# Performance work log

Hardware: AMD Instinct MI355X
Metric: run time of the kernel (lower is better)

## Reference

```python
import jax, jax.numpy as jnp
import numpy as np

D_MODEL = 1024
H = 16
D_K = D_MODEL // H  # 64
B, S = 2, 2048


def setup_inputs() -> dict:
    key = jax.random.key(0)
    ks = jax.random.split(key, 8)
    scale = 1.0 / np.sqrt(D_MODEL)
    return {
        "q": jax.random.normal(ks[0], (B, S, D_MODEL), dtype=jnp.float32),
        "k": jax.random.normal(ks[1], (B, S, D_MODEL), dtype=jnp.float32),
        "v": jax.random.normal(ks[2], (B, S, D_MODEL), dtype=jnp.float32),
        "W_q": jax.random.normal(ks[3], (H, D_MODEL, D_K), dtype=jnp.float32) * scale,
        "W_k": jax.random.normal(ks[4], (H, D_MODEL, D_K), dtype=jnp.float32) * scale,
        "W_v": jax.random.normal(ks[5], (H, D_MODEL, D_K), dtype=jnp.float32) * scale,
        "W_o": jax.random.normal(ks[6], (D_MODEL, H * D_K), dtype=jnp.float32) * scale,
        "b_o": jnp.zeros((D_MODEL,), dtype=jnp.float32),
    }


def reference(q, k, v, W_q, W_k, W_v, W_o, b_o):
    b, s, _ = q.shape
    h, _, d_k = W_q.shape
    inv_sqrt_dk = jnp.asarray(1.0 / np.sqrt(d_k), q.dtype)
    # per-head projections: [b, h, s, d_k]
    qh = jnp.einsum("bsd,hdk->bhsk", q, W_q)
    kh = jnp.einsum("bsd,hdk->bhsk", k, W_k)
    vh = jnp.einsum("bsd,hdk->bhsk", v, W_v)
    # scaled dot product attention
    scores = jnp.einsum("bhqk,bhsk->bhqs", qh, kh) * inv_sqrt_dk  # [b,h,S,S]
    attn = jax.nn.softmax(scores, axis=-1)
    ctx = jnp.einsum("bhqs,bhsk->bhqk", attn, vh)  # [b,h,S,d_k]
    # chunk over heads + concat along feature dim -> [b, S, h*d_k], head-major
    ctx = ctx.transpose(0, 2, 1, 3).reshape(b, s, h * d_k)
    # final linear
    return ctx @ W_o.T + b_o
```

## Files before the change

### kernel.cpp

```cpp
#include <hip/hip_runtime.h>
#include <cstdint>
#include <cstddef>


typedef unsigned short bf16_t;
typedef __attribute__((ext_vector_type(8))) short short8;
typedef __attribute__((ext_vector_type(4))) float f32x4;
typedef __attribute__((ext_vector_type(16))) float f32x16;
typedef __attribute__((ext_vector_type(2))) unsigned int uint2v;

__device__ __forceinline__ uint32_t fbits(float f) {
  union { float f; uint32_t u; } v; v.f = f; return v.u;
}
__device__ __forceinline__ bf16_t f2bf(float f) {
  uint32_t u = fbits(f);
  return (bf16_t)((u + 0x7FFFu + ((u >> 16) & 1u)) >> 16);
}
__device__ __forceinline__ uint32_t packbf2(float lo, float hi) {
  uint32_t a = fbits(hi) + 0x8000u;
  uint32_t b = fbits(lo) + 0x8000u;
  return __builtin_amdgcn_perm(a, b, 0x07060302u);
}
__device__ __forceinline__ int4 cvt8(f32x4 lo, f32x4 hi) {
  return make_int4((int)packbf2(lo.x, lo.y), (int)packbf2(lo.z, lo.w),
                   (int)packbf2(hi.x, hi.y), (int)packbf2(hi.z, hi.w));
}

__device__ __forceinline__ void gload16(const bf16_t* g, bf16_t* l) {
  __builtin_amdgcn_global_load_lds(
      (const __attribute__((address_space(1))) void*)g,
      (__attribute__((address_space(3))) void*)l, 16, 0, 0);
}

__global__ void prep_kernel(const float* __restrict__ Wo,
                            const float* __restrict__ Wq, const float* __restrict__ Wk,
                            const float* __restrict__ Wv,
                            const float* __restrict__ q, const float* __restrict__ k,
                            const float* __restrict__ v,
                            bf16_t* __restrict__ Woo,
                            bf16_t* __restrict__ Wtq, bf16_t* __restrict__ Wtk,
                            bf16_t* __restrict__ Wtv,
                            bf16_t* __restrict__ qb, bf16_t* __restrict__ kb,
                            bf16_t* __restrict__ vb) {
  int blk = blockIdx.x;
  int tid = threadIdx.x;
  if (blk < 1024) {
    int i = blk * 256 + tid;
    f32x4 val = ((const f32x4*)Wo)[i];
    ushort4 o;
    o.x = f2bf(val.x); o.y = f2bf(val.y); o.z = f2bf(val.z); o.w = f2bf(val.w);
    ((ushort4*)Woo)[i] = o;
  } else if (blk < 2560) {
    int blk2 = blk - 1024;
    int z = blk2 >> 9, t = blk2 & 511;
    const float* W = z == 0 ? Wq : z == 1 ? Wk : Wv;
    bf16_t* Wt = z == 0 ? Wtq : z == 1 ? Wtk : Wtv;
    int h = t >> 5, d0 = (t & 31) * 32;
    __shared__ float tile[32][65];
    const float* src = W + ((size_t)h << 16) + (size_t)d0 * 64;
    int d = tid >> 3;
#pragma unroll
    for (int j = 0; j < 2; j++) {
      int dk = (tid & 7) * 8 + j * 4;
      *(f32x4*)&tile[d][dk] = *(const f32x4*)(src + d * 64 + dk);
    }
    __syncthreads();
    int dk2 = tid >> 2, c = tid & 3;
    union { ushort s[8]; int4 v; } o;
#pragma unroll
    for (int j = 0; j < 8; j++) o.s[j] = f2bf(tile[c * 8 + j][dk2]);
    *(int4*)(Wt + (size_t)(h * 64 + dk2) * 1024 + d0 + c * 8) = o.v;
  } else {
    int blk3 = blk - 2560;
    int z = blk3 >> 11;
    int t3 = blk3 & 2047;
    const float* src = z == 0 ? q : z == 1 ? k : v;
    bf16_t* dst = z == 0 ? qb : z == 1 ? kb : vb;
    int i = t3 * 256 + tid;
    f32x4 lo = ((const f32x4*)src)[i * 2];
    f32x4 hi = ((const f32x4*)src)[i * 2 + 1];
    ((int4*)dst)[i] = cvt8(lo, hi);
  }
}

__global__ __launch_bounds__(256) void gemm_proj_kernel(
    const bf16_t* __restrict__ A0, const bf16_t* __restrict__ A1, const bf16_t* __restrict__ A2,
    const bf16_t* __restrict__ B0, const bf16_t* __restrict__ B1, const bf16_t* __restrict__ B2,
    bf16_t* __restrict__ O0, bf16_t* __restrict__ O1, bf16_t* __restrict__ O2,
    float s0)
{
  const int bid = blockIdx.x;
  const int nIdx = bid / 96;
  const int g = bid - nIdx * 96;
  const int z = g % 3;
  const int m0 = (g / 3) * 128, n0 = nIdx * 128;

  const bf16_t* A  = z == 0 ? A0 : z == 1 ? A1 : A2;
  const bf16_t* Bt = z == 0 ? B0 : z == 1 ? B1 : B2;
  bf16_t* Cout     = z == 0 ? O0 : z == 1 ? O1 : O2;
  const float scale = z == 0 ? s0 : 1.0f;
  const int K = 1024;

  __shared__ alignas(16) bf16_t smem[18432];

  const int tid = threadIdx.x;
  const int lane = tid & 63, wave = tid >> 6;
  const int wm = wave >> 1, wn = wave & 1;
  const int quad = lane >> 4, l15 = lane & 15;

  f32x4 acc[4][4];
#pragma unroll
  for (int i = 0; i < 4; i++)
#pragma unroll
    for (int j = 0; j < 4; j++) acc[i][j] = (f32x4)0.0f;

  const int srow = tid >> 2, scol = (tid & 3) * 8;
  const bf16_t* pa0 = A  + (size_t)(m0 + srow) * K + scol;
  const bf16_t* pa1 = pa0 + (size_t)64 * K;
  const bf16_t* pb0 = Bt + (size_t)(n0 + srow) * K + scol;
  const bf16_t* pb1 = pb0 + (size_t)64 * K;
  const int lws = wave * 512;

  gload16(pa0, smem + lws);
  gload16(pa1, smem + 2048 + lws);
  gload16(pb0, smem + 4096 + lws);
  gload16(pb1, smem + 6144 + lws);
  __syncthreads();

  for (int it = 0; it < 32; ++it) {
    const int cur = (it & 1) * 8192;
    if (it < 31) {
      const int nxt = ((it + 1) & 1) * 8192;
      const int ko = (it + 1) * 32;
      gload16(pa0 + ko, smem + nxt + lws);
      gload16(pa1 + ko, smem + nxt + 2048 + lws);
      gload16(pb0 + ko, smem + nxt + 4096 + lws);
      gload16(pb1 + ko, smem + nxt + 6144 + lws);
    }

    short8 af[4], bfr[4];
#pragma unroll
    for (int mi = 0; mi < 4; mi++)
      af[mi] = *(const short8*)(smem + cur + (wm * 64 + mi * 16 + l15) * 32 + quad * 8);
#pragma unroll
    for (int ni = 0; ni < 4; ni++)
      bfr[ni] = *(const short8*)(smem + cur + 4096 + (wn * 64 + ni * 16 + l15) * 32 + quad * 8);
#pragma unroll
    for (int mi = 0; mi < 4; mi++)
#pragma unroll
      for (int ni = 0; ni < 4; ni++)
        acc[mi][ni] = __builtin_amdgcn_mfma_f32_16x16x32_bf16(af[mi], bfr[ni], acc[mi][ni], 0, 0, 0);

    __syncthreads();
  }

  const int s0r = m0 & 2047, bb = m0 >> 11, hp = n0 >> 6;
  if (z < 2) {
    bf16_t* slot = smem + wn * 9216;
#pragma unroll
    for (int ni = 0; ni < 4; ni++)
#pragma unroll
      for (int mi = 0; mi < 4; mi++)
#pragma unroll
        for (int r = 0; r < 4; r++)
          slot[(wm * 64 + mi * 16 + quad * 4 + r) * 72 + ni * 16 + l15] =
              f2bf(acc[mi][ni][r] * scale);
    __syncthreads();
#pragma unroll
    for (int rd = 0; rd < 8; ++rd) {
      int idx = rd * 256 + tid;
      int si = idx >> 10, mm = (idx >> 3) & 127, c8 = idx & 7;
      int4 val = *(const int4*)(smem + si * 9216 + mm * 72 + c8 * 8);
      size_t head = (size_t)(bb * 16 + hp + si);
      if (z == 0) {
        *(int4*)(Cout + (head * 2048 + s0r + mm) * 64 + c8 * 8) = val;
      } else {
        int row = s0r + mm;
        int tile = row >> 6, loc = row & 63;
        int f = (loc >> 5) * 4 + (c8 >> 1);
        int j = (c8 & 1) * 32 + (loc & 31);
        *(int4*)(Cout + head * 131072 + (size_t)tile * 4096 + f * 512 + j * 8) = val;
      }
    }
  } else {
    bf16_t* slot = smem + wn * 8704;
#pragma unroll
    for (int ni = 0; ni < 4; ni++)
#pragma unroll
      for (int mi = 0; mi < 4; mi++) {
        uint2 pk = make_uint2(packbf2(acc[mi][ni][0], acc[mi][ni][1]),
                              packbf2(acc[mi][ni][2], acc[mi][ni][3]));
        *(uint2*)(slot + (ni * 16 + l15) * 136 + wm * 64 + mi * 16 + quad * 4) = pk;
      }
    __syncthreads();
#pragma unroll
    for (int rd = 0; rd < 8; ++rd) {
      int idx = rd * 256 + tid;
      int si = idx >> 10, c = (idx >> 4) & 63, ck = idx & 15;
      int4 val = *(const int4*)(smem + si * 8704 + c * 136 + ck * 8);
      int kk = s0r + ck * 8;
      int tile = kk >> 6;
      int f = (c >> 5) * 4 + ((kk >> 4) & 3);
      int j = ((kk >> 3) & 1) * 32 + (c & 31);
      *(int4*)(Cout + (size_t)(bb * 16 + hp + si) * 131072 + (size_t)tile * 4096 + f * 512 + j * 8) = val;
    }
  }
}

__global__ __launch_bounds__(256) void gemm_out_kernel(
    const bf16_t* __restrict__ A, const bf16_t* __restrict__ Bt,
    float* __restrict__ C, const float* __restrict__ bias)
{
  const int K = 1024, N = 1024;
  __shared__ alignas(16) bf16_t smem[12288];
  const int tid = threadIdx.x;
  const int lane = tid & 63, wave = tid >> 6;
  const int quad = lane >> 4, l15 = lane & 15;
  const int m0 = (blockIdx.x & 31) * 128, n0 = (blockIdx.x >> 5) * 64;

  f32x4 acc[2][4];
#pragma unroll
  for (int i = 0; i < 2; i++)
#pragma unroll
    for (int j = 0; j < 4; j++) acc[i][j] = (f32x4)0.0f;

  const int srow = tid >> 2, scol = (tid & 3) * 8;
  const bf16_t* pa0 = A  + (size_t)(m0 + srow) * K + scol;
  const bf16_t* pa1 = pa0 + (size_t)64 * K;
  const bf16_t* pb  = Bt + (size_t)(n0 + srow) * K + scol;
  const int lws = wave * 512;

  gload16(pa0, smem + lws);
  gload16(pa1, smem + 2048 + lws);
  gload16(pb,  smem + 4096 + lws);
  __syncthreads();

  for (int it = 0; it < 32; ++it) {
    const int cur = (it & 1) * 6144;
    if (it < 31) {
      const int nxt = ((it + 1) & 1) * 6144;
      const int ko = (it + 1) * 32;
      gload16(pa0 + ko, smem + nxt + lws);
      gload16(pa1 + ko, smem + nxt + 2048 + lws);
      gload16(pb + ko,  smem + nxt + 4096 + lws);
    }

    short8 af[2], bfr[4];
#pragma unroll
    for (int mi = 0; mi < 2; mi++)
      af[mi] = *(const short8*)(smem + cur + (wave * 32 + mi * 16 + l15) * 32 + quad * 8);
#pragma unroll
    for (int ni = 0; ni < 4; ni++)
      bfr[ni] = *(const short8*)(smem + cur + 4096 + (ni * 16 + l15) * 32 + quad * 8);
#pragma unroll
    for (int mi = 0; mi < 2; mi++)
#pragma unroll
      for (int ni = 0; ni < 4; ni++)
        acc[mi][ni] = __builtin_amdgcn_mfma_f32_16x16x32_bf16(af[mi], bfr[ni], acc[mi][ni], 0, 0, 0);

    __syncthreads();
  }

#pragma unroll
  for (int ni = 0; ni < 4; ni++) {
    int col = n0 + ni * 16 + l15;
    float bv = bias[col];
#pragma unroll
    for (int mi = 0; mi < 2; mi++) {
      int row = m0 + wave * 32 + mi * 16 + quad * 4;
#pragma unroll
      for (int r = 0; r < 4; r++)
        C[(size_t)(row + r) * N + col] = acc[mi][ni][r] + bv;
    }
  }
}

__global__ __launch_bounds__(256) void flash_kernel(
    const bf16_t* __restrict__ qh, const bf16_t* __restrict__ kh,
    const bf16_t* __restrict__ vh, bf16_t* __restrict__ ctx)
{
  __shared__ alignas(16) bf16_t smem[16384];
  const int tid = threadIdx.x, lane = tid & 63, wave = tid >> 6;
  const int hlf = lane >> 5, l31 = lane & 31;
  const int gid = blockIdx.x;
  const int hb = gid & 31;
  const int h = hb & 15, b = hb >> 4;
  const int q0 = (gid >> 5) * 128;
  const size_t headoff = (size_t)hb * 131072;
  const bf16_t* Q  = qh + headoff;
  const bf16_t* Kf = kh + headoff;
  const bf16_t* Vf = vh + headoff;

  short8 qf[4];
#pragma unroll
  for (int dk = 0; dk < 4; dk++)
    qf[dk] = *(const short8*)(Q + (size_t)(q0 + wave * 32 + l31) * 64 + dk * 16 + hlf * 8);

  f32x16 Oa = (f32x16)0.0f, Ob = (f32x16)0.0f;
  float lsum = 0.0f;

  const bf16_t* Kp0 = Kf + tid * 8;
  const bf16_t* Kp1 = Kf + tid * 8 + 2048;
  const bf16_t* Vp0 = Vf + 4096 - 4096 + tid * 8;
  const bf16_t* Vp1 = Vf + tid * 8 + 2048;
  bf16_t* sK = smem + tid * 8;
  bf16_t* sV = smem + 4096 + tid * 8;

  auto body = [&](int buf) {
    const bf16_t* Kb = smem + buf * 8192;
    const bf16_t* Vb = smem + buf * 8192 + 4096;
    f32x16 S0 = (f32x16)0.0f, S1 = (f32x16)0.0f;
#pragma unroll
    for (int dk = 0; dk < 4; dk++) {
      short8 kf0 = *(const short8*)(Kb + dk * 512 + lane * 8);
      short8 kf1 = *(const short8*)(Kb + (4 + dk) * 512 + lane * 8);
      S0 = __builtin_amdgcn_mfma_f32_32x32x16_bf16(kf0, qf[dk], S0, 0, 0, 0);
      S1 = __builtin_amdgcn_mfma_f32_32x32x16_bf16(kf1, qf[dk], S1, 0, 0, 0);
    }
#pragma unroll
    for (int r = 0; r < 16; r++) {
      S0[r] = __builtin_amdgcn_exp2f(S0[r]);
      S1[r] = __builtin_amdgcn_exp2f(S1[r]);
    }
    {
      f32x16 ss = S0 + S1;
      float a0 = (ss[0] + ss[1]) + (ss[2] + ss[3]);
      float a1 = (ss[4] + ss[5]) + (ss[6] + ss[7]);
      float a2 = (ss[8] + ss[9]) + (ss[10] + ss[11]);
      float a3 = (ss[12] + ss[13]) + (ss[14] + ss[15]);
      lsum += (a0 + a1) + (a2 + a3);
    }
#pragma unroll
    for (int mi = 0; mi < 2; mi++) {
      f32x16 P = mi ? S1 : S0;
#pragma unroll
      for (int ksl = 0; ksl < 2; ksl++) {
        const int ks = mi * 2 + ksl, base = ksl * 8;
        uint32_t X = packbf2(P[base + 0], P[base + 1]);
        uint32_t Y = packbf2(P[base + 2], P[base + 3]);
        uint32_t Z = packbf2(P[base + 4], P[base + 5]);
        uint32_t W = packbf2(P[base + 6], P[base + 7]);
        uint2v r1 = __builtin_amdgcn_permlane32_swap(X, Z, false, false);
        uint2v r2 = __builtin_amdgcn_permlane32_swap(Y, W, false, false);
        int4 bi = make_int4((int)r1.x, (int)r2.x, (int)r1.y, (int)r2.y);
        short8 Bf = *(short8*)&bi;
        short8 vf0 = *(const short8*)(Vb + ks * 512 + lane * 8);
        short8 vf1 = *(const short8*)(Vb + (4 + ks) * 512 + lane * 8);
        Oa = __builtin_amdgcn_mfma_f32_32x32x16_bf16(vf0, Bf, Oa, 0, 0, 0);
        Ob = __builtin_amdgcn_mfma_f32_32x32x16_bf16(vf1, Bf, Ob, 0, 0, 0);
      }
    }
  };

  int4 k0a = *(const int4*)Kp0, k0b = *(const int4*)Kp1;
  int4 v0a = *(const int4*)Vp0, v0b = *(const int4*)Vp1;
  *(int4*)sK = k0a; *(int4*)(sK + 2048) = k0b;
  *(int4*)sV = v0a; *(int4*)(sV + 2048) = v0b;
  int4 kAa = *(const int4*)(Kp0 + 4096), kAb = *(const int4*)(Kp1 + 4096);
  int4 vAa = *(const int4*)(Vp0 + 4096), vAb = *(const int4*)(Vp1 + 4096);
  __syncthreads();

  for (int it = 0; it < 32; it += 2) {
    *(int4*)(sK + 8192) = kAa; *(int4*)(sK + 8192 + 2048) = kAb;
    *(int4*)(sV + 8192) = vAa; *(int4*)(sV + 8192 + 2048) = vAb;
    int4 kBa, kBb, vBa, vBb;
    if (it + 2 < 32) {
      kBa = *(const int4*)(Kp0 + (size_t)(it + 2) * 4096);
      kBb = *(const int4*)(Kp1 + (size_t)(it + 2) * 4096);
      vBa = *(const int4*)(Vp0 + (size_t)(it + 2) * 4096);
      vBb = *(const int4*)(Vp1 + (size_t)(it + 2) * 4096);
    }
    body(0);
    __syncthreads();

    if (it + 2 < 32) {
      *(int4*)sK = kBa; *(int4*)(sK + 2048) = kBb;
      *(int4*)sV = vBa; *(int4*)(sV + 2048) = vBb;
    }
    if (it + 3 < 32) {
      kAa = *(const int4*)(Kp0 + (size_t)(it + 3) * 4096);
      kAb = *(const int4*)(Kp1 + (size_t)(it + 3) * 4096);
      vAa = *(const int4*)(Vp0 + (size_t)(it + 3) * 4096);
      vAb = *(const int4*)(Vp1 + (size_t)(it + 3) * 4096);
    }
    body(1);
    __syncthreads();
  }

  lsum += __shfl_xor(lsum, 32, 64);
  float inv = 1.0f / lsum;
  bf16_t* slot = smem + wave * 2048;
  const int swz = l31 & 7;
#pragma unroll
  for (int dmi = 0; dmi < 2; dmi++) {
    f32x16 Ov = dmi ? Ob : Oa;
#pragma unroll
    for (int rq = 0; rq < 4; rq++) {
      uint2 pk = make_uint2(packbf2(Ov[rq * 4 + 0] * inv, Ov[rq * 4 + 1] * inv),
                            packbf2(Ov[rq * 4 + 2] * inv, Ov[rq * 4 + 3] * inv));
      int c = dmi * 4 + rq;
      *(uint2*)(slot + l31 * 64 + ((c ^ swz) * 8 + 4 * hlf)) = pk;
    }
  }
  __syncthreads();
#pragma unroll
  for (int p = 0; p < 4; p++) {
    int s2 = p * 64 + lane;
    int qr = s2 >> 3, cr = s2 & 7;
    int4 val = *(const int4*)(slot + qr * 64 + ((cr ^ (qr & 7)) * 8));
    *(int4*)(ctx + (size_t)(b * 2048 + q0 + wave * 32 + qr) * 1024 + h * 64 + cr * 8) = val;
  }
}

extern "C" void kernel_launch(void* const* d_in, const int* in_sizes, int n_in,
                              void* d_out, int out_size, void* d_ws, size_t ws_size,
                              hipStream_t stream)
{
  const float* q  = (const float*)d_in[0];
  const float* k  = (const float*)d_in[1];
  const float* v  = (const float*)d_in[2];
  const float* Wq = (const float*)d_in[3];
  const float* Wk = (const float*)d_in[4];
  const float* Wv = (const float*)d_in[5];
  const float* Wo = (const float*)d_in[6];
  const float* bo = (const float*)d_in[7];
  float* out = (float*)d_out;

  const size_t NX = (size_t)4096 * 1024;
  const size_t NW = (size_t)1024 * 1024;

  char* p = (char*)d_ws;
  bf16_t* Wtq = (bf16_t*)p; p += NW * 2;
  bf16_t* Wtk = (bf16_t*)p; p += NW * 2;
  bf16_t* Wtv = (bf16_t*)p; p += NW * 2;
  bf16_t* Wob = (bf16_t*)p; p += NW * 2;
  bf16_t* qb  = (bf16_t*)p; p += NX * 2;
  bf16_t* kb  = (bf16_t*)p; p += NX * 2;
  bf16_t* vb  = (bf16_t*)p; p += NX * 2;
  bf16_t* qhb = (bf16_t*)p; p += NX * 2;
  bf16_t* khb = (bf16_t*)p; p += NX * 2;
  bf16_t* vTb = (bf16_t*)p; p += NX * 2;
  bf16_t* ctxb = (bf16_t*)p; p += NX * 2;

  prep_kernel<<<8704, 256, 0, stream>>>(Wo, Wq, Wk, Wv, q, k, v,
                                        Wob, Wtq, Wtk, Wtv, qb, kb, vb);

  const float qscale = 0.125f * 1.44269504088896340736f;
  gemm_proj_kernel<<<768, 256, 0, stream>>>(qb, kb, vb, Wtq, Wtk, Wtv,
                                            qhb, khb, vTb, qscale);

  flash_kernel<<<512, 256, 0, stream>>>(qhb, khb, vTb, ctxb);

  gemm_out_kernel<<<512, 256, 0, stream>>>(ctxb, Wob, out, bo);

  (void)in_sizes; (void)n_in; (void)out_size; (void)ws_size;
}
```

Before: 212.3 us.

## Software-pipeline QK^T of next tile with softmax and PV of current tile

Restructures the flash attention inner loop so that the QK^T MFMAs for tile t+1 are issued alongside the exp/softmax and PV MFMAs for tile t. K keeps a double buffer while V moves to a triple buffer with rotating indices, which raises LDS use to 40KB. The goal is to hide exp2 and pack latency behind matrix work. In exchange it holds two extra f32x16 score accumulators, raising register pressure and possibly lowering occupancy.

```diff
diff --git a/kernel.cpp b/kernel.cpp
--- a/kernel.cpp
+++ b/kernel.cpp
@@ -279,7 +279,7 @@
     const bf16_t* __restrict__ qh, const bf16_t* __restrict__ kh,
     const bf16_t* __restrict__ vh, bf16_t* __restrict__ ctx)
 {
-  __shared__ alignas(16) bf16_t smem[16384];
+  __shared__ alignas(16) bf16_t smem[20480];
   const int tid = threadIdx.x, lane = tid & 63, wave = tid >> 6;
   const int hlf = lane >> 5, l31 = lane & 31;
   const int gid = blockIdx.x;
@@ -297,19 +297,18 @@
     qf[dk] = *(const short8*)(Q + (size_t)(q0 + wave * 32 + l31) * 64 + dk * 16 + hlf * 8);
 
   f32x16 Oa = (f32x16)0.0f, Ob = (f32x16)0.0f;
+  f32x16 SA0, SA1, SB0, SB1;
   float lsum = 0.0f;
 
   const bf16_t* Kp0 = Kf + tid * 8;
   const bf16_t* Kp1 = Kf + tid * 8 + 2048;
-  const bf16_t* Vp0 = Vf + 4096 - 4096 + tid * 8;
+  const bf16_t* Vp0 = Vf + tid * 8;
   const bf16_t* Vp1 = Vf + tid * 8 + 2048;
-  bf16_t* sK = smem + tid * 8;
-  bf16_t* sV = smem + 4096 + tid * 8;
-
-  auto body = [&](int buf) {
-    const bf16_t* Kb = smem + buf * 8192;
-    const bf16_t* Vb = smem + buf * 8192 + 4096;
-    f32x16 S0 = (f32x16)0.0f, S1 = (f32x16)0.0f;
+  bf16_t* const sKw = smem + tid * 8;
+  bf16_t* const sVw = smem + 8192 + tid * 8;
+
+  auto qk = [&](f32x16& S0, f32x16& S1, const bf16_t* Kb) {
+    S0 = (f32x16)0.0f; S1 = (f32x16)0.0f;
 #pragma unroll
     for (int dk = 0; dk < 4; dk++) {
       short8 kf0 = *(const short8*)(Kb + dk * 512 + lane * 8);
@@ -317,6 +316,9 @@
       S0 = __builtin_amdgcn_mfma_f32_32x32x16_bf16(kf0, qf[dk], S0, 0, 0, 0);
       S1 = __builtin_amdgcn_mfma_f32_32x32x16_bf16(kf1, qf[dk], S1, 0, 0, 0);
     }
+  };
+
+  auto softpv = [&](f32x16& S0, f32x16& S1, const bf16_t* Vb) {
 #pragma unroll
     for (int r = 0; r < 16; r++) {
       S0[r] = __builtin_amdgcn_exp2f(S0[r]);
@@ -332,7 +334,7 @@
     }
 #pragma unroll
     for (int mi = 0; mi < 2; mi++) {
-      f32x16 P = mi ? S1 : S0;
+      const f32x16& P = mi ? S1 : S0;
 #pragma unroll
       for (int ksl = 0; ksl < 2; ksl++) {
         const int ks = mi * 2 + ksl, base = ksl * 8;
@@ -352,40 +354,53 @@
     }
   };
 
-  int4 k0a = *(const int4*)Kp0, k0b = *(const int4*)Kp1;
-  int4 v0a = *(const int4*)Vp0, v0b = *(const int4*)Vp1;
-  *(int4*)sK = k0a; *(int4*)(sK + 2048) = k0b;
-  *(int4*)sV = v0a; *(int4*)(sV + 2048) = v0b;
+  {
+    int4 k0a = *(const int4*)Kp0, k0b = *(const int4*)Kp1;
+    int4 v0a = *(const int4*)Vp0, v0b = *(const int4*)Vp1;
+    *(int4*)sKw = k0a; *(int4*)(sKw + 2048) = k0b;
+    *(int4*)sVw = v0a; *(int4*)(sVw + 2048) = v0b;
+  }
   int4 kAa = *(const int4*)(Kp0 + 4096), kAb = *(const int4*)(Kp1 + 4096);
   int4 vAa = *(const int4*)(Vp0 + 4096), vAb = *(const int4*)(Vp1 + 4096);
   __syncthreads();
 
-  for (int it = 0; it < 32; it += 2) {
-    *(int4*)(sK + 8192) = kAa; *(int4*)(sK + 8192 + 2048) = kAb;
-    *(int4*)(sV + 8192) = vAa; *(int4*)(sV + 8192 + 2048) = vAb;
-    int4 kBa, kBb, vBa, vBb;
-    if (it + 2 < 32) {
-      kBa = *(const int4*)(Kp0 + (size_t)(it + 2) * 4096);
-      kBb = *(const int4*)(Kp1 + (size_t)(it + 2) * 4096);
-      vBa = *(const int4*)(Vp0 + (size_t)(it + 2) * 4096);
-      vBb = *(const int4*)(Vp1 + (size_t)(it + 2) * 4096);
-    }
-    body(0);
-    __syncthreads();
-
-    if (it + 2 < 32) {
-      *(int4*)sK = kBa; *(int4*)(sK + 2048) = kBb;
-      *(int4*)sV = vBa; *(int4*)(sV + 2048) = vBb;
-    }
-    if (it + 3 < 32) {
-      kAa = *(const int4*)(Kp0 + (size_t)(it + 3) * 4096);
-      kAb = *(const int4*)(Kp1 + (size_t)(it + 3) * 4096);
-      vAa = *(const int4*)(Vp0 + (size_t)(it + 3) * 4096);
-      vAb = *(const int4*)(Vp1 + (size_t)(it + 3) * 4096);
-    }
-    body(1);
-    __syncthreads();
-  }
+  *(int4*)(sKw + 4096) = kAa; *(int4*)(sKw + 4096 + 2048) = kAb;
+  *(int4*)(sVw + 4096) = vAa; *(int4*)(sVw + 4096 + 2048) = vAb;
+  int4 kBa = *(const int4*)(Kp0 + 8192), kBb = *(const int4*)(Kp1 + 8192);
+  int4 vBa = *(const int4*)(Vp0 + 8192), vBb = *(const int4*)(Vp1 + 8192);
+  qk(SA0, SA1, smem);
+  __syncthreads();
+
+  int m0 = 0, m1 = 1, m2 = 2;
+  for (int t = 1; t < 31; t += 2) {
+    *(int4*)sKw = kBa; *(int4*)(sKw + 2048) = kBb;
+    *(int4*)(sVw + m2 * 4096) = vBa; *(int4*)(sVw + m2 * 4096 + 2048) = vBb;
+    {
+      const size_t ko = (size_t)(t + 2) * 4096;
+      kAa = *(const int4*)(Kp0 + ko); kAb = *(const int4*)(Kp1 + ko);
+      vAa = *(const int4*)(Vp0 + ko); vAb = *(const int4*)(Vp1 + ko);
+    }
+    qk(SB0, SB1, smem + 4096);
+    softpv(SA0, SA1, smem + 8192 + m0 * 4096);
+    __syncthreads();
+
+    *(int4*)(sKw + 4096) = kAa; *(int4*)(sKw + 4096 + 2048) = kAb;
+    *(int4*)(sVw + m0 * 4096) = vAa; *(int4*)(sVw + m0 * 4096 + 2048) = vAb;
+    if (t + 3 < 32) {
+      const size_t ko = (size_t)(t + 3) * 4096;
+      kBa = *(const int4*)(Kp0 + ko); kBb = *(const int4*)(Kp1 + ko);
+      vBa = *(const int4*)(Vp0 + ko); vBb = *(const int4*)(Vp1 + ko);
+    }
+    qk(SA0, SA1, smem);
+    softpv(SB0, SB1, smem + 8192 + m1 * 4096);
+    __syncthreads();
+
+    int tmp = m2; m2 = m1; m1 = m0; m0 = tmp;
+  }
+  qk(SB0, SB1, smem + 4096);
+  softpv(SA0, SA1, smem + 8192 + m0 * 4096);
+  __syncthreads();
+  softpv(SB0, SB1, smem + 8192 + m1 * 4096);
 
   lsum += __shfl_xor(lsum, 32, 64);
   float inv = 1.0f / lsum;
@@ -393,7 +408,7 @@
   const int swz = l31 & 7;
 #pragma unroll
   for (int dmi = 0; dmi < 2; dmi++) {
-    f32x16 Ov = dmi ? Ob : Oa;
+    const f32x16& Ov = dmi ? Ob : Oa;
 #pragma unroll
     for (int rq = 0; rq < 4; rq++) {
       uint2 pk = make_uint2(packbf2(Ov[rq * 4 + 0] * inv, Ov[rq * 4 + 1] * inv),
```

New measurement: 209.6 us. About the same (-1.2%).
